# Performance work log

Measured on AMD Instinct MI355X. Metric: run time of the kernel, lower is better.

Reference implementation:

```python
import jax, jax.numpy as jnp
import numpy as np

DIM, N_HEADS, N_KV, HEAD_DIM = 4096, 32, 8, 128
REPEATS = N_HEADS // N_KV
SCALE = HEAD_DIM ** -0.5


def apply_rope(x, offset=0):
    # x: [b, h, l, hd]; rotation convention matches the torch source:
    # out_even = xe*cos + xo*sin, out_odd = -xe*sin + xo*cos, interleaved back.
    hd = x.shape[-1]
    l = x.shape[2]
    freqs = 1.0 / 10000.0 ** (jnp.arange(0, hd, 2, dtype=jnp.float32) / hd)  # [hd/2]
    t = jnp.arange(l, dtype=jnp.float32) + offset
    ang = t[:, None] * freqs[None, :]                     # [l, hd/2]
    sin, cos = jnp.sin(ang), jnp.cos(ang)
    xe, xo = x[..., 0::2], x[..., 1::2]                   # [b,h,l,hd/2]
    out = jnp.stack([xe * cos + xo * sin, -xe * sin + xo * cos], axis=-1)
    return out.reshape(x.shape)


def setup_inputs() -> dict:
    key = jax.random.key(0)
    ks = jax.random.split(key, 5)
    b, l = 1, 2048
    x = jax.random.normal(ks[0], (b, l, DIM), dtype=jnp.float32)
    # additive causal mask: 0 on/below diagonal, -1e9 above
    neg = jnp.full((l, l), -1e9, dtype=jnp.float32)
    mask = jnp.triu(neg, k=1)
    wq = jax.random.normal(ks[1], (N_HEADS * HEAD_DIM, DIM), dtype=jnp.float32) * 0.02
    wk = jax.random.normal(ks[2], (N_KV * HEAD_DIM, DIM), dtype=jnp.float32) * 0.02
    wv = jax.random.normal(ks[3], (N_KV * HEAD_DIM, DIM), dtype=jnp.float32) * 0.02
    wo = jax.random.normal(ks[4], (DIM, N_HEADS * HEAD_DIM), dtype=jnp.float32) * 0.02
    return {"x": x, "mask": mask, "wq": wq, "wk": wk, "wv": wv, "wo": wo}


def reference(x, mask, wq, wk, wv, wo):
    b, l, d = x.shape
    q = (x @ wq.T).reshape(b, l, N_HEADS, HEAD_DIM).transpose(0, 2, 1, 3)  # [b,H,l,hd]
    k = (x @ wk.T).reshape(b, l, N_KV, HEAD_DIM).transpose(0, 2, 1, 3)     # [b,Hk,l,hd]
    v = (x @ wv.T).reshape(b, l, N_KV, HEAD_DIM).transpose(0, 2, 1, 3)
    # GQA repeat (head = kv_head*repeats + r, same as torch cat+view)
    k = jnp.repeat(k, REPEATS, axis=1)
    v = jnp.repeat(v, REPEATS, axis=1)
    q = apply_rope(q)
    k = apply_rope(k)
    atn = jnp.einsum('bhqd,bhkd->bhqk', q * SCALE, k) + mask
    atn = jax.nn.softmax(atn.astype(jnp.float32), axis=-1).astype(q.dtype)
    out = jnp.einsum('bhqk,bhkd->bhqd', atn, v)
    out = out.transpose(0, 2, 1, 3).reshape(b, l, -1)
    return (out @ wo.T, k, v)
```

## Files before the change

kernel.cpp:

```cpp
#include <hip/hip_runtime.h>
#include <stdint.h>

#define L_SEQ  2048
#define NHEAD  32
#define NKV    8
#define HD     128
#define DIM    4096
#define KVDIM  1024
#define QKVS   6144
#define SCALE  0.08838834764831845f
#define LOG2E  1.4426950408889634f
#define SM_OFF 12.0f

typedef __attribute__((ext_vector_type(8))) short bf16x8;
typedef __attribute__((ext_vector_type(4))) float f32x4;

#define FENCE() asm volatile("" ::: "memory")

__device__ __forceinline__ unsigned short f2bf(float f) {
    unsigned u = __float_as_uint(f);
    u = (u + 0x7FFFu + ((u >> 16) & 1u)) >> 16;
    return (unsigned short)u;
}
__device__ __forceinline__ float bf2f(unsigned short h) {
    return __uint_as_float(((unsigned)h) << 16);
}
__device__ __forceinline__ void gload_lds16(const void* g, void* l) {
    __builtin_amdgcn_global_load_lds(
        (const __attribute__((address_space(1))) unsigned int*)g,
        (__attribute__((address_space(3))) unsigned int*)l, 16, 0, 0);
}

__global__ void cvt_f32_bf16(const float* __restrict__ in, unsigned short* __restrict__ out, int n4) {
    int i = blockIdx.x * blockDim.x + threadIdx.x;
    int stride = gridDim.x * blockDim.x;
    for (; i < n4; i += stride) {
        float4 v = ((const float4*)in)[i];
        ushort4 o;
        o.x = f2bf(v.x); o.y = f2bf(v.y); o.z = f2bf(v.z); o.w = f2bf(v.w);
        ((ushort4*)out)[i] = o;
    }
}

__global__ void addf32(float* __restrict__ out, const float* __restrict__ p, int n4) {
    int i = blockIdx.x * blockDim.x + threadIdx.x;
    int stride = gridDim.x * blockDim.x;
    for (; i < n4; i += stride) {
        float4 a = ((const float4*)out)[i];
        float4 b = ((const float4*)p)[i];
        a.x += b.x; a.y += b.y; a.z += b.z; a.w += b.w;
        ((float4*)out)[i] = a;
    }
}

__global__ void rope_table(float2* __restrict__ rt) {
    int i = blockIdx.x * blockDim.x + threadIdx.x;
    if (i >= L_SEQ * 64) return;
    int l = i >> 6, f = i & 63;
    float freq = powf(10000.0f, -(float)f / 64.0f);
    float ang  = (float)l * freq;
    rt[i] = make_float2(cosf(ang), sinf(ang));
}

__global__ void rope_apply(unsigned short* __restrict__ X, const float2* __restrict__ rt,
                           int log2H, int strideShorts, float mul) {
    int i = blockIdx.x * blockDim.x + threadIdx.x;
    int f  = i & 63;
    int hh = (i >> 6) & ((1 << log2H) - 1);
    int l  = i >> (6 + log2H);
    if (l >= L_SEQ) return;
    float2 cs = rt[(l << 6) + f];
    size_t base = (size_t)l * strideShorts + (hh << 7);
    float xe = bf2f(X[base + 2 * f]);
    float xo = bf2f(X[base + 2 * f + 1]);
    X[base + 2 * f]     = f2bf((xe * cs.x + xo * cs.y) * mul);
    X[base + 2 * f + 1] = f2bf((-xe * cs.y + xo * cs.x) * mul);
}

__global__ void kv_out(const unsigned short* __restrict__ KVp,
                       float* __restrict__ KO, float* __restrict__ VO) {
    int i = blockIdx.x * blockDim.x + threadIdx.x;
    if (i >= L_SEQ * KVDIM) return;
    int d  = i & 127;
    int h8 = (i >> 7) & 7;
    int l  = i >> 10;
    float kv = bf2f(KVp[(size_t)l * QKVS + h8 * HD + d]);
    float vv = bf2f(KVp[(size_t)l * QKVS + KVDIM + h8 * HD + d]);
#pragma unroll
    for (int r = 0; r < 4; ++r) {
        int h = h8 * 4 + r;
        KO[((size_t)h * L_SEQ + l) * HD + d] = kv;
        VO[((size_t)h * L_SEQ + l) * HD + d] = vv;
    }
}

__global__ void vtrans(const unsigned short* __restrict__ KVp, unsigned short* __restrict__ VT) {
    __shared__ unsigned short t[32][33];
    int lt = blockIdx.x * 32;
    int h8 = blockIdx.y >> 2;
    int dt = (blockIdx.y & 3) * 32;
    int tx = threadIdx.x & 31, ty = threadIdx.x >> 5;
#pragma unroll
    for (int yy = ty; yy < 32; yy += 8)
        t[yy][tx] = KVp[(size_t)(lt + yy) * QKVS + KVDIM + h8 * HD + dt + tx];
    __syncthreads();
#pragma unroll
    for (int yy = ty; yy < 32; yy += 8)
        VT[(size_t)(h8 * HD + dt + yy) * L_SEQ + lt + tx] = t[tx][yy];
}

template <typename OT, int NF>
__global__ __launch_bounds__(512, 2) void gemm_8ph(const unsigned short* __restrict__ A,
                                                   const unsigned short* __restrict__ B,
                                                   OT* __restrict__ C0, OT* __restrict__ C1,
                                                   int N, int K, int klen) {
    __shared__ __align__(16) char L[65536 + 2 * NF * 8192];
    const int tid = threadIdx.x;
    const int w = tid >> 6, lane = tid & 63;
    const int gx = gridDim.x;
    const int nwg = gx * gridDim.y;
    const int orig = blockIdx.y * gx + blockIdx.x;
    const int swz = (orig & 7) * (nwg >> 3) + (orig >> 3);
    const int m0 = (swz / gx) * 256, n0 = (swz % gx) * (NF * 64);
    const int kbase = blockIdx.z * klen;
    OT* __restrict__ C = blockIdx.z ? C1 : C0;
    const int wr = (w >> 2) & 1;
    const int wc = w & 3;
    const int lr = lane & 15, lg = lane >> 4;
    const int NKT = klen >> 6;
    const int swb = (lr & 7) << 4;

    auto stageA = [&](int slot, int u, int kt) {
        int r  = u * 64 + w * 8 + (lane >> 3);
        int cg = (lane & 7) ^ (r & 7);
        gload_lds16(A + (size_t)(m0 + r) * K + kbase + kt * 64 + cg * 8,
                    L + slot * 32768 + (u * 64 + w * 8) * 128);
    };
    auto stageB = [&](int slot, int u, int kt) {
        int r  = u * 64 + w * 8 + (lane >> 3);
        int cg = (lane & 7) ^ (r & 7);
        gload_lds16(B + (size_t)(n0 + r) * K + kbase + kt * 64 + cg * 8,
                    L + 65536 + slot * (NF * 8192) + (u * 64 + w * 8) * 128);
    };

    const f32x4 fz = {0.f, 0.f, 0.f, 0.f};
    f32x4 acc[8][NF];
#pragma unroll
    for (int m = 0; m < 8; ++m)
#pragma unroll
        for (int n = 0; n < NF; ++n) acc[m][n] = fz;

    bf16x8 bfr[NF][2];

#pragma unroll
    for (int u = 0; u < 4; ++u) stageA(0, u, 0);
#pragma unroll
    for (int u = 0; u < NF; ++u) stageB(0, u, 0);
    if (NKT > 1) {
#pragma unroll
        for (int u = 0; u < NF; ++u) stageB(1, u, 1);
    }
    if constexpr (NF == 4) asm volatile("s_waitcnt vmcnt(4)" ::: "memory");
    else                   asm volatile("s_waitcnt vmcnt(3)" ::: "memory");
    __builtin_amdgcn_s_barrier();
    FENCE();

    for (int kt0 = 0; kt0 < NKT; kt0 += 2) {
#pragma unroll
        for (int kp = 0; kp < 2; ++kp) {
            const int kt = kt0 + kp;
            const int s = kp;
            const char* Abase = L + s * 32768;
            const char* Bbase = L + 65536 + s * (NF * 8192);
#pragma unroll
            for (int q = 0; q < 4; ++q) {
                bf16x8 af[2][2];
#pragma unroll
                for (int mm = 0; mm < 2; ++mm)
#pragma unroll
                    for (int kk = 0; kk < 2; ++kk) {
                        int r = wr * 128 + (q * 2 + mm) * 16 + lr;
                        int b = (kk * 64 + lg * 16) ^ swb;
                        af[mm][kk] = *(const bf16x8*)(Abase + r * 128 + b);
                    }
                if (q == 0) {
#pragma unroll
                    for (int n = 0; n < NF; ++n)
#pragma unroll
                        for (int kk = 0; kk < 2; ++kk) {
                            int r = wc * (NF * 16) + n * 16 + lr;
                            int b = (kk * 64 + lg * 16) ^ swb;
                            bfr[n][kk] = *(const bf16x8*)(Bbase + r * 128 + b);
                        }
                }
                if (q == 0 && kt + 1 < NKT) { stageA(s ^ 1, 0, kt + 1); stageA(s ^ 1, 1, kt + 1); }
                if (q == 1 && kt + 1 < NKT) { stageA(s ^ 1, 2, kt + 1); stageA(s ^ 1, 3, kt + 1); }
                if (q == 2 && kt + 2 < NKT) { stageB(s, 0, kt + 2); stageB(s, 1, kt + 2); }
                if (q == 3) {
                    if (kt + 2 < NKT) {
                        stageB(s, 2, kt + 2);
                        if constexpr (NF == 4) {
                            stageB(s, 3, kt + 2);
                            asm volatile("s_waitcnt vmcnt(4)" ::: "memory");
                        } else {
                            asm volatile("s_waitcnt vmcnt(3)" ::: "memory");
                        }
                    } else {
                        asm volatile("s_waitcnt vmcnt(0)" ::: "memory");
                    }
                }
                FENCE();
                __builtin_amdgcn_s_barrier();
                FENCE();
                __builtin_amdgcn_s_setprio(1);
#pragma unroll
                for (int mm = 0; mm < 2; ++mm)
#pragma unroll
                    for (int n = 0; n < NF; ++n)
#pragma unroll
                        for (int kk = 0; kk < 2; ++kk)
                            acc[q * 2 + mm][n] = __builtin_amdgcn_mfma_f32_16x16x32_bf16(
                                af[mm][kk], bfr[n][kk], acc[q * 2 + mm][n], 0, 0, 0);
                __builtin_amdgcn_s_setprio(0);
                FENCE();
                __builtin_amdgcn_s_barrier();
                FENCE();
            }
        }
    }
#pragma unroll
    for (int m = 0; m < 8; ++m) {
        int mrow = m0 + wr * 128 + m * 16 + lg * 4;
#pragma unroll
        for (int n = 0; n < NF; ++n) {
            int ncol = n0 + wc * (NF * 16) + n * 16 + lr;
#pragma unroll
            for (int r = 0; r < 4; ++r) {
                float v = acc[m][n][r];
                if constexpr (sizeof(OT) == 2) C[(size_t)(mrow + r) * N + ncol] = f2bf(v);
                else                           C[(size_t)(mrow + r) * N + ncol] = v;
            }
        }
    }
}

__global__ __launch_bounds__(128) void attn_fwd(const unsigned short* __restrict__ Q,
                                                const unsigned short* __restrict__ KVp,
                                                const unsigned short* __restrict__ VT,
                                                unsigned short* __restrict__ AO) {
    __shared__ __align__(16) unsigned short Ks[64 * 128];
    __shared__ __align__(16) unsigned short Vs[128 * 64];
    __shared__ __align__(16) unsigned short P[2][2][16][64];
    const int tid = threadIdx.x, w = tid >> 6, lane = tid & 63;
    const int idx = blockIdx.x;
    const int h8  = idx & 7;
    const int h   = (h8 << 2) + ((idx >> 3) & 3);
    const int u   = idx >> 5;
    const int t   = u & 7, quart = u >> 3;
    const int qb  = (quart == 0) ? 31 - t : (quart == 1) ? 16 + t
                  : (quart == 2) ? 15 - t : t;
    const int lr = lane & 15, lg = lane >> 4;
    const int r0 = qb * 64 + w * 32;

    bf16x8 qf[2][4];
#pragma unroll
    for (int f = 0; f < 2; ++f) {
        const unsigned short* qrow = Q + (size_t)(r0 + f * 16 + lr) * QKVS + h * HD + lg * 8;
#pragma unroll
        for (int kd = 0; kd < 4; ++kd) qf[f][kd] = *(const bf16x8*)(qrow + kd * 32);
    }

    bf16x8 ones;
#pragma unroll
    for (int z = 0; z < 8; ++z) ones[z] = (short)0x3F80;

    const f32x4 fz = {0.f, 0.f, 0.f, 0.f};
    f32x4 o[2][9];
#pragma unroll
    for (int f = 0; f < 2; ++f)
#pragma unroll
        for (int nd = 0; nd < 9; ++nd) o[f][nd] = fz;

    const int nkv = qb + 1;
    for (int kv = 0; kv < nkv; ++kv) {
        const int kv0 = kv * 64;
#pragma unroll
        for (int c = 0; c < 8; ++c) {
            int krow = w * 32 + c * 4 + (lane >> 4);
            int kcg  = (lane & 15) ^ (krow & 7);
            gload_lds16(KVp + (size_t)(kv0 + krow) * QKVS + h8 * HD + kcg * 8,
                        Ks + (w * 32 + c * 4) * 128);
            int vrow = w * 64 + c * 8 + (lane >> 3);
            int vcg  = (lane & 7) ^ (vrow & 7);
            gload_lds16(VT + (size_t)(h8 * HD + vrow) * L_SEQ + kv0 + vcg * 8,
                        Vs + (w * 64 + c * 8) * 64);
        }
        __syncthreads();
        f32x4 s[2][4];
#pragma unroll
        for (int f = 0; f < 2; ++f)
#pragma unroll
            for (int ni = 0; ni < 4; ++ni) s[f][ni] = fz;
        __builtin_amdgcn_s_setprio(1);
#pragma unroll
        for (int ni = 0; ni < 4; ++ni) {
            bf16x8 kf[4];
#pragma unroll
            for (int kd = 0; kd < 4; ++kd)
                kf[kd] = *(const bf16x8*)(Ks + (ni * 16 + lr) * 128 +
                                          (((kd * 4 + lg) ^ (lr & 7)) * 8));
#pragma unroll
            for (int f = 0; f < 2; ++f)
#pragma unroll
                for (int kd = 0; kd < 4; ++kd)
                    s[f][ni] = __builtin_amdgcn_mfma_f32_16x16x32_bf16(qf[f][kd], kf[kd], s[f][ni], 0, 0, 0);
        }
        __builtin_amdgcn_s_setprio(0);
#pragma unroll
        for (int f = 0; f < 2; ++f) {
            const int rbase = r0 + f * 16;
            const bool need_mask = (kv0 + 63) > rbase;
#pragma unroll
            for (int ni = 0; ni < 4; ++ni)
#pragma unroll
                for (int rr = 0; rr < 4; ++rr) {
                    float p = __builtin_amdgcn_exp2f(s[f][ni][rr] - SM_OFF);
                    if (need_mask) {
                        int col = kv0 + ni * 16 + lr;
                        int row = rbase + lg * 4 + rr;
                        p = (col > row) ? 0.f : p;
                    }
                    s[f][ni][rr] = p;
                }
            char* Pb = (char*)&P[w][f][0][0];
#pragma unroll
            for (int ni = 0; ni < 4; ni += 2)
#pragma unroll
                for (int rr = 0; rr < 4; ++rr) {
                    unsigned pk;
                    asm("v_cvt_pk_bf16_f32 %0, %1, %2" : "=v"(pk) : "v"(s[f][ni][rr]), "v"(s[f][ni + 1][rr]));
                    const int row = lg * 4 + rr;
                    const int sw = (row & 7) << 4;
                    *(unsigned short*)(Pb + ((row * 128 + (ni * 16 + lr) * 2) ^ sw)) = (unsigned short)pk;
                    *(unsigned short*)(Pb + ((row * 128 + ((ni + 1) * 16 + lr) * 2) ^ sw)) =
                        (unsigned short)(pk >> 16);
                }
        }
        bf16x8 pa[2][2];
        const int swr = (lr & 7) << 4;
#pragma unroll
        for (int f = 0; f < 2; ++f) {
            const char* Pb = (const char*)&P[w][f][0][0];
#pragma unroll
            for (int ks = 0; ks < 2; ++ks)
                pa[f][ks] = *(const bf16x8*)(Pb + ((lr * 128 + ks * 64 + lg * 16) ^ swr));
        }
        __builtin_amdgcn_s_setprio(1);
#pragma unroll
        for (int nd = 0; nd < 8; ++nd) {
            bf16x8 vf[2];
#pragma unroll
            for (int ks = 0; ks < 2; ++ks)
                vf[ks] = *(const bf16x8*)(Vs + (nd * 16 + lr) * 64 +
                                          (((ks * 4 + lg) ^ (lr & 7)) * 8));
#pragma unroll
            for (int f = 0; f < 2; ++f)
#pragma unroll
                for (int ks = 0; ks < 2; ++ks)
                    o[f][nd] = __builtin_amdgcn_mfma_f32_16x16x32_bf16(pa[f][ks], vf[ks], o[f][nd], 0, 0, 0);
        }
#pragma unroll
        for (int f = 0; f < 2; ++f)
#pragma unroll
            for (int ks = 0; ks < 2; ++ks)
                o[f][8] = __builtin_amdgcn_mfma_f32_16x16x32_bf16(pa[f][ks], ones, o[f][8], 0, 0, 0);
        __builtin_amdgcn_s_setprio(0);
        __syncthreads();
    }
#pragma unroll
    for (int f = 0; f < 2; ++f) {
        float inv[4];
#pragma unroll
        for (int rr = 0; rr < 4; ++rr) inv[rr] = 1.0f / o[f][8][rr];
#pragma unroll
        for (int nd = 0; nd < 8; ++nd)
#pragma unroll
            for (int rr = 0; rr < 4; ++rr) {
                int row = r0 + f * 16 + lg * 4 + rr;
                AO[(size_t)row * DIM + h * HD + nd * 16 + lr] = f2bf(o[f][nd][rr] * inv[rr]);
            }
    }
}

extern "C" void kernel_launch(void* const* d_in, const int* in_sizes, int n_in,
                              void* d_out, int out_size, void* d_ws, size_t ws_size,
                              hipStream_t stream) {
    (void)in_sizes; (void)n_in; (void)out_size; (void)ws_size;
    const float* x  = (const float*)d_in[0];
    const float* wq = (const float*)d_in[2];
    const float* wk = (const float*)d_in[3];
    const float* wv = (const float*)d_in[4];
    const float* wo = (const float*)d_in[5];

    float* out = (float*)d_out;
    float* KO  = out + (size_t)L_SEQ * DIM;
    float* VO  = KO + (size_t)NHEAD * L_SEQ * HD;

    char* ws = (char*)d_ws;
    const size_t MB = 1024 * 1024;
    unsigned short* xb   = (unsigned short*)(ws);
    unsigned short* wqb  = (unsigned short*)(ws + 16 * MB);
    unsigned short* wkvb = (unsigned short*)(ws + 48 * MB);
    unsigned short* qkvp = (unsigned short*)(ws + 64 * MB);
    unsigned short* vtb  = (unsigned short*)(ws + 88 * MB);
    float2*         rt   = (float2*)(ws + 92 * MB);
    unsigned short* aob  = xb;
    unsigned short* wob  = wqb;
    unsigned short* kvp  = qkvp + KVDIM * 4;
    float*          pko  = (float*)(ws + 48 * MB);

    cvt_f32_bf16<<<2048, 256, 0, stream>>>(x,  xb,  L_SEQ * DIM / 4);
    cvt_f32_bf16<<<2048, 256, 0, stream>>>(wq, wqb, DIM * DIM / 4);
    cvt_f32_bf16<<<2048, 256, 0, stream>>>(wk, wkvb, KVDIM * DIM / 4);
    cvt_f32_bf16<<<2048, 256, 0, stream>>>(wv, wkvb + (size_t)KVDIM * DIM, KVDIM * DIM / 4);
    rope_table<<<(L_SEQ * 64) / 256, 256, 0, stream>>>(rt);

    gemm_8ph<unsigned short, 3><<<dim3(QKVS / 192, L_SEQ / 256, 1), 512, 0, stream>>>(
        xb, wqb, qkvp, qkvp, QKVS, DIM, DIM);
    cvt_f32_bf16<<<2048, 256, 0, stream>>>(wo, wob, DIM * DIM / 4);

    rope_apply<<<(L_SEQ * NHEAD * 64) / 256, 256, 0, stream>>>(qkvp, rt, 5, QKVS, SCALE * LOG2E);
    rope_apply<<<(L_SEQ * NKV * 64) / 256, 256, 0, stream>>>(kvp, rt, 3, QKVS, 1.0f);

    kv_out<<<(L_SEQ * KVDIM) / 256, 256, 0, stream>>>(kvp, KO, VO);
    vtrans<<<dim3(L_SEQ / 32, 32), 256, 0, stream>>>(kvp, vtb);

    attn_fwd<<<1024, 128, 0, stream>>>(qkvp, kvp, vtb, aob);

    gemm_8ph<float, 4><<<dim3(DIM / 256, L_SEQ / 256, 2), 512, 0, stream>>>(
        aob, wob, out, pko, DIM, DIM, DIM / 2);
    addf32<<<2048, 256, 0, stream>>>(out, pko, L_SEQ * DIM / 4);
}
```

Baseline: 333.0 us.

## Overlap K/V tile loads with compute in attention and fuse V output into vtrans

The attention loop now splits K and V staging. The next K tile is issued after QK^T finishes and the next V tile after PV finishes, with vmcnt waits and raw barriers in place of full syncthreads, so global-to-LDS loads overlap the softmax and MFMA work. The fp32 V output write moves from kv_out into the vtrans kernel, which already reads V, so V is read from global memory only once. The risks are extra barriers per iteration and a redundant prefetch of tile 0 on the last iteration.

```diff
diff --git a/kernel.cpp b/kernel.cpp
--- a/kernel.cpp
+++ b/kernel.cpp
@@ -77,32 +77,34 @@
     X[base + 2 * f + 1] = f2bf((-xe * cs.y + xo * cs.x) * mul);
 }
 
-__global__ void kv_out(const unsigned short* __restrict__ KVp,
-                       float* __restrict__ KO, float* __restrict__ VO) {
+__global__ void kv_out(const unsigned short* __restrict__ KVp, float* __restrict__ KO) {
     int i = blockIdx.x * blockDim.x + threadIdx.x;
     if (i >= L_SEQ * KVDIM) return;
     int d  = i & 127;
     int h8 = (i >> 7) & 7;
     int l  = i >> 10;
     float kv = bf2f(KVp[(size_t)l * QKVS + h8 * HD + d]);
-    float vv = bf2f(KVp[(size_t)l * QKVS + KVDIM + h8 * HD + d]);
-#pragma unroll
-    for (int r = 0; r < 4; ++r) {
-        int h = h8 * 4 + r;
-        KO[((size_t)h * L_SEQ + l) * HD + d] = kv;
-        VO[((size_t)h * L_SEQ + l) * HD + d] = vv;
-    }
-}
-
-__global__ void vtrans(const unsigned short* __restrict__ KVp, unsigned short* __restrict__ VT) {
+#pragma unroll
+    for (int r = 0; r < 4; ++r)
+        KO[((size_t)(h8 * 4 + r) * L_SEQ + l) * HD + d] = kv;
+}
+
+__global__ void vtrans(const unsigned short* __restrict__ KVp, unsigned short* __restrict__ VT,
+                       float* __restrict__ VO) {
     __shared__ unsigned short t[32][33];
     int lt = blockIdx.x * 32;
     int h8 = blockIdx.y >> 2;
     int dt = (blockIdx.y & 3) * 32;
     int tx = threadIdx.x & 31, ty = threadIdx.x >> 5;
 #pragma unroll
-    for (int yy = ty; yy < 32; yy += 8)
-        t[yy][tx] = KVp[(size_t)(lt + yy) * QKVS + KVDIM + h8 * HD + dt + tx];
+    for (int yy = ty; yy < 32; yy += 8) {
+        unsigned short v = KVp[(size_t)(lt + yy) * QKVS + KVDIM + h8 * HD + dt + tx];
+        t[yy][tx] = v;
+        float vf = bf2f(v);
+#pragma unroll
+        for (int r = 0; r < 4; ++r)
+            VO[((size_t)(h8 * 4 + r) * L_SEQ + lt + yy) * HD + dt + tx] = vf;
+    }
     __syncthreads();
 #pragma unroll
     for (int yy = ty; yy < 32; yy += 8)
@@ -262,40 +264,55 @@
     const int lr = lane & 15, lg = lane >> 4;
     const int r0 = qb * 64 + w * 32;
 
-    bf16x8 qf[2][4];
-#pragma unroll
-    for (int f = 0; f < 2; ++f) {
-        const unsigned short* qrow = Q + (size_t)(r0 + f * 16 + lr) * QKVS + h * HD + lg * 8;
-#pragma unroll
-        for (int kd = 0; kd < 4; ++kd) qf[f][kd] = *(const bf16x8*)(qrow + kd * 32);
-    }
-
-    bf16x8 ones;
-#pragma unroll
-    for (int z = 0; z < 8; ++z) ones[z] = (short)0x3F80;
-
-    const f32x4 fz = {0.f, 0.f, 0.f, 0.f};
-    f32x4 o[2][9];
-#pragma unroll
-    for (int f = 0; f < 2; ++f)
-#pragma unroll
-        for (int nd = 0; nd < 9; ++nd) o[f][nd] = fz;
-
-    const int nkv = qb + 1;
-    for (int kv = 0; kv < nkv; ++kv) {
-        const int kv0 = kv * 64;
+    auto stageK = [&](int kvb) {
 #pragma unroll
         for (int c = 0; c < 8; ++c) {
             int krow = w * 32 + c * 4 + (lane >> 4);
             int kcg  = (lane & 15) ^ (krow & 7);
-            gload_lds16(KVp + (size_t)(kv0 + krow) * QKVS + h8 * HD + kcg * 8,
+            gload_lds16(KVp + (size_t)(kvb * 64 + krow) * QKVS + h8 * HD + kcg * 8,
                         Ks + (w * 32 + c * 4) * 128);
+        }
+    };
+    auto stageV = [&](int kvb) {
+#pragma unroll
+        for (int c = 0; c < 8; ++c) {
             int vrow = w * 64 + c * 8 + (lane >> 3);
             int vcg  = (lane & 7) ^ (vrow & 7);
-            gload_lds16(VT + (size_t)(h8 * HD + vrow) * L_SEQ + kv0 + vcg * 8,
+            gload_lds16(VT + (size_t)(h8 * HD + vrow) * L_SEQ + kvb * 64 + vcg * 8,
                         Vs + (w * 64 + c * 8) * 64);
         }
-        __syncthreads();
+    };
+
+    bf16x8 qf[2][4];
+#pragma unroll
+    for (int f = 0; f < 2; ++f) {
+        const unsigned short* qrow = Q + (size_t)(r0 + f * 16 + lr) * QKVS + h * HD + lg * 8;
+#pragma unroll
+        for (int kd = 0; kd < 4; ++kd) qf[f][kd] = *(const bf16x8*)(qrow + kd * 32);
+    }
+
+    bf16x8 ones;
+#pragma unroll
+    for (int z = 0; z < 8; ++z) ones[z] = (short)0x3F80;
+
+    const f32x4 fz = {0.f, 0.f, 0.f, 0.f};
+    f32x4 o[2][9];
+#pragma unroll
+    for (int f = 0; f < 2; ++f)
+#pragma unroll
+        for (int nd = 0; nd < 9; ++nd) o[f][nd] = fz;
+
+    const int nkv = qb + 1;
+    stageK(0);
+    stageV(0);
+
+    for (int kv = 0; kv < nkv; ++kv) {
+        const int kv0 = kv * 64;
+        const int kvn = (kv + 1 < nkv) ? kv + 1 : 0;
+        asm volatile("s_waitcnt vmcnt(8)" ::: "memory");
+        FENCE();
+        __builtin_amdgcn_s_barrier();
+        FENCE();
         f32x4 s[2][4];
 #pragma unroll
         for (int f = 0; f < 2; ++f)
@@ -316,6 +333,10 @@
                     s[f][ni] = __builtin_amdgcn_mfma_f32_16x16x32_bf16(qf[f][kd], kf[kd], s[f][ni], 0, 0, 0);
         }
         __builtin_amdgcn_s_setprio(0);
+        FENCE();
+        __builtin_amdgcn_s_barrier();
+        FENCE();
+        stageK(kvn);
 #pragma unroll
         for (int f = 0; f < 2; ++f) {
             const int rbase = r0 + f * 16;
@@ -346,6 +367,10 @@
                         (unsigned short)(pk >> 16);
                 }
         }
+        asm volatile("s_waitcnt vmcnt(8)" ::: "memory");
+        FENCE();
+        __builtin_amdgcn_s_barrier();
+        FENCE();
         bf16x8 pa[2][2];
         const int swr = (lr & 7) << 4;
 #pragma unroll
@@ -375,7 +400,10 @@
             for (int ks = 0; ks < 2; ++ks)
                 o[f][8] = __builtin_amdgcn_mfma_f32_16x16x32_bf16(pa[f][ks], ones, o[f][8], 0, 0, 0);
         __builtin_amdgcn_s_setprio(0);
-        __syncthreads();
+        FENCE();
+        __builtin_amdgcn_s_barrier();
+        FENCE();
+        stageV(kvn);
     }
 #pragma unroll
     for (int f = 0; f < 2; ++f) {
@@ -432,8 +460,8 @@
     rope_apply<<<(L_SEQ * NHEAD * 64) / 256, 256, 0, stream>>>(qkvp, rt, 5, QKVS, SCALE * LOG2E);
     rope_apply<<<(L_SEQ * NKV * 64) / 256, 256, 0, stream>>>(kvp, rt, 3, QKVS, 1.0f);
 
-    kv_out<<<(L_SEQ * KVDIM) / 256, 256, 0, stream>>>(kvp, KO, VO);
-    vtrans<<<dim3(L_SEQ / 32, 32), 256, 0, stream>>>(kvp, vtb);
+    kv_out<<<(L_SEQ * KVDIM) / 256, 256, 0, stream>>>(kvp, KO);
+    vtrans<<<dim3(L_SEQ / 32, 32), 256, 0, stream>>>(kvp, vtb, VO);
 
     attn_fwd<<<1024, 128, 0, stream>>>(qkvp, kvp, vtb, aob);
 
```

Measured after the change: 344.6 us. +3.5%, slower.
